# Kernel tuning notes

Measured on AMD Instinct MI355X. Metric: run time of the kernel, lower is better.

## Reference

```python
import jax, jax.numpy as jnp
import numpy as np

N, E, R, B, IN, H, OUT, P = 20000, 320000, 8, 8, 128, 256, 128, 100000
LN_EPS = 1e-5


def _xavier(key, shape):
    fan_in, fan_out = shape[-2], shape[-1]
    lim = float(np.sqrt(6.0 / (fan_in + fan_out)))
    return jax.random.uniform(key, shape, jnp.float32, -lim, lim)


def setup_inputs() -> dict:
    key = jax.random.key(0)
    ks = iter(jax.random.split(key, 64))
    inp = {}
    inp['x'] = jax.random.normal(next(ks), (N, IN), jnp.float32)
    inp['edge_index'] = jax.random.randint(next(ks), (2, E), 0, N, jnp.int32)
    inp['edge_type'] = jax.random.randint(next(ks), (E,), 0, R, jnp.int32)
    inp['gene_pairs'] = jax.random.randint(next(ks), (2, P), 0, N, jnp.int32)
    dims = [(IN, H), (H, H), (H, H), (H, OUT)]  # per-layer (in_ch, out_ch)
    for i, (ic, oc) in enumerate(dims):
        inp[f'basis{i}'] = _xavier(next(ks), (B, ic, oc))
        inp[f'att{i}'] = _xavier(next(ks), (R, B))
        inp[f'root{i}'] = _xavier(next(ks), (ic, oc))
        inp[f'relatt{i}'] = jnp.ones((R,), jnp.float32)
        inp[f'g{i}'] = jnp.ones((oc,), jnp.float32)
        inp[f'b{i}'] = jnp.zeros((oc,), jnp.float32)
    inp['res0'] = _xavier(next(ks), (IN, H))   # in_ch != out_ch at layer 0
    inp['res3'] = _xavier(next(ks), (H, OUT))  # and at layer 3
    # decoder: 3*OUT -> H -> H//2 -> H//4 -> 1
    ddims = [(3 * OUT, H), (H, H // 2), (H // 2, H // 4), (H // 4, 1)]
    for i, (ic, oc) in enumerate(ddims):
        inp[f'dW{i}'] = _xavier(next(ks), (ic, oc))
        inp[f'db{i}'] = jnp.zeros((oc,), jnp.float32)
        if i < 3:
            inp[f'dg{i}'] = jnp.ones((oc,), jnp.float32)
            inp[f'dbb{i}'] = jnp.zeros((oc,), jnp.float32)
    return inp


def _ln(h, g, b):
    m = h.mean(-1, keepdims=True)
    v = ((h - m) ** 2).mean(-1, keepdims=True)
    return (h - m) * jax.lax.rsqrt(v + LN_EPS) * g + b


def _conv(x, src, dst, et, basis, att, root_w, rel_att):
    # W_r = sum_b att[r,b] * B_b ; message = a_{r(e)} * x_src @ W_{r(e)}
    # Since the message is linear, aggregate x_src per (dst, relation) first
    # (segment_sum), then apply the R small GEMMs once - same math, no [E,in,out].
    n, d = x.shape
    weight = jnp.einsum('rb,bio->rio', att, basis)          # [R,in,out]
    a = jax.nn.softmax(rel_att)                              # [R]
    seg = dst.astype(jnp.int32) * R + et.astype(jnp.int32)   # [(node,rel)] segment ids
    agg = jax.ops.segment_sum(x[src], seg, num_segments=n * R).reshape(n, R, d)
    out = jnp.einsum('nri,rio->no', agg, weight * a[:, None, None])
    return out + x @ root_w


def reference(x, edge_index, edge_type, gene_pairs,
              basis0, att0, root0, relatt0, g0, b0, res0,
              basis1, att1, root1, relatt1, g1, b1,
              basis2, att2, root2, relatt2, g2, b2,
              basis3, att3, root3, relatt3, g3, b3, res3,
              dW0, db0, dg0, dbb0, dW1, db1, dg1, dbb1,
              dW2, db2, dg2, dbb2, dW3, db3):
    src, dst = edge_index[0], edge_index[1]
    layers = [
        (basis0, att0, root0, relatt0, g0, b0, res0),
        (basis1, att1, root1, relatt1, g1, b1, None),
        (basis2, att2, root2, relatt2, g2, b2, None),
        (basis3, att3, root3, relatt3, g3, b3, res3),
    ]
    h = x
    for i, (bs, at, rt, ra, g, b, res) in enumerate(layers):
        h_in = h
        h = _conv(h, src, dst, edge_type, bs, at, rt, ra)
        h = _ln(h, g, b)
        h = h + (h_in @ res if res is not None else h_in)
        if i < len(layers) - 1:
            h = jax.nn.gelu(h, approximate=False)
    z = h  # [N, OUT]
    zi, zj = z[gene_pairs[0]], z[gene_pairs[1]]
    pe = jnp.concatenate([zi + zj, zi * zj, jnp.abs(zi - zj)], axis=-1)
    d = jax.nn.gelu(_ln(pe @ dW0 + db0, dg0, dbb0), approximate=False)
    d = jax.nn.gelu(_ln(d @ dW1 + db1, dg1, dbb1), approximate=False)
    d = jax.nn.gelu(_ln(d @ dW2 + db2, dg2, dbb2), approximate=False)
    logits = (d @ dW3 + db3).squeeze(-1)  # [P]
    return logits, z
```

## Files before the change

### kernel.cpp

```cpp
#include <hip/hip_runtime.h>
#include <hip/hip_bf16.h>
#include <math.h>
#include <cstddef>
#include <stdint.h>

#define NN 20000
#define EE 320000
#define RR 8
#define PP 100000
#define NR (NN * RR)

typedef __hip_bfloat16 bf16;
typedef __attribute__((ext_vector_type(8))) short short8;
typedef __attribute__((ext_vector_type(4))) float floatx4;

__device__ __forceinline__ float b2f(bf16 v) { return __bfloat162float(v); }
__device__ __forceinline__ bf16 f2b(float v) { return __float2bfloat16(v); }
__device__ __forceinline__ float bits2f(unsigned short u) {
  unsigned int i = ((unsigned int)u) << 16; float f; __builtin_memcpy(&f, &i, 4); return f;
}
__device__ __forceinline__ short f2bits(float f) {
  bf16 h = __float2bfloat16(f); short s; __builtin_memcpy(&s, &h, 2); return s;
}
__device__ __forceinline__ float gelu_f(float y) {
  return 0.5f * y * (1.f + erff(y * 0.7071067811865476f));
}
__device__ __forceinline__ void async_copy16(void* lds, const void* g) {
  __builtin_amdgcn_global_load_lds((const __attribute__((address_space(1))) void*)g,
                                   (__attribute__((address_space(3))) void*)lds, 16, 0, 0);
}
__device__ __forceinline__ const short8* frag_at(const bf16* base, int row, int q) {
  return (const short8*)(base + row * 64 + (((q) ^ (row & 7)) << 3));
}
__device__ __forceinline__ const short8* frag256(const bf16* base, int row, int col64, int q) {
  return (const short8*)(base + row * 256 + col64 + (((q) ^ (row & 7)) << 3));
}
__device__ __forceinline__ int idx128(int row, int qg) {
  return row * 128 + ((qg >> 3) << 6) + (((qg & 7) ^ (row & 7)) << 3);
}

__global__ void hist_k(const int* __restrict__ dst, const int* __restrict__ et,
                       int* __restrict__ counts) {
  int e = blockIdx.x * 256 + threadIdx.x;
  if (e >= EE) return;
  atomicAdd(&counts[dst[e] * RR + et[e]], 1);
}

__global__ void scan1_k(const int* __restrict__ counts, int* __restrict__ prefix,
                        int* __restrict__ bsums) {
  __shared__ int tmp[256];
  int i = blockIdx.x * 256 + threadIdx.x;
  int v = counts[i];
  tmp[threadIdx.x] = v; __syncthreads();
  for (int off = 1; off < 256; off <<= 1) {
    int x = (threadIdx.x >= off) ? tmp[threadIdx.x - off] : 0;
    __syncthreads();
    tmp[threadIdx.x] += x;
    __syncthreads();
  }
  prefix[i] = tmp[threadIdx.x] - v;
  if (threadIdx.x == 255) bsums[blockIdx.x] = tmp[255];
}

__global__ void scan2_k(int* __restrict__ bsums, int nb) {
  __shared__ int tmp[256];
  __shared__ int carry;
  if (threadIdx.x == 0) carry = 0;
  __syncthreads();
  for (int base = 0; base < nb; base += 256) {
    int i = base + threadIdx.x;
    int v = (i < nb) ? bsums[i] : 0;
    tmp[threadIdx.x] = v; __syncthreads();
    for (int off = 1; off < 256; off <<= 1) {
      int x = (threadIdx.x >= off) ? tmp[threadIdx.x - off] : 0;
      __syncthreads();
      tmp[threadIdx.x] += x;
      __syncthreads();
    }
    int c = carry;
    if (i < nb) bsums[i] = c + tmp[threadIdx.x] - v;
    __syncthreads();
    if (threadIdx.x == 255) carry = c + tmp[255];
    __syncthreads();
  }
}

__global__ void scan3_k(int* __restrict__ prefix, const int* __restrict__ bsums) {
  int i = blockIdx.x * 256 + threadIdx.x;
  prefix[i] += bsums[blockIdx.x];
}

__global__ void scatter_k(const int* __restrict__ src, const int* __restrict__ dst,
                          const int* __restrict__ et, const int* __restrict__ segstart,
                          int* __restrict__ cursor, int* __restrict__ ssrc) {
  int e = blockIdx.x * 256 + threadIdx.x;
  if (e >= EE) return;
  int s = dst[e] * RR + et[e];
  int pos = atomicAdd(&cursor[s], 1);
  ssrc[segstart[s] + pos] = src[e];
}

__global__ void cvt_bf16_k(const float* __restrict__ in, bf16* __restrict__ out, int n) {
  int i = blockIdx.x * 256 + threadIdx.x;
  if (i < n) out[i] = f2b(in[i]);
}

__global__ void softmax4_k(const float* r0, const float* r1, const float* r2,
                           const float* r3, float* __restrict__ a) {
  if (threadIdx.x == 0) {
    const float* rs[4] = {r0, r1, r2, r3};
    for (int l = 0; l < 4; ++l) {
      float mx = -1e30f;
      for (int i = 0; i < RR; ++i) mx = fmaxf(mx, rs[l][i]);
      float e[RR]; float s = 0.f;
      for (int i = 0; i < RR; ++i) { e[i] = expf(rs[l][i] - mx); s += e[i]; }
      for (int i = 0; i < RR; ++i) a[l * RR + i] = e[i] / s;
    }
  }
}

__global__ void transpose_k(const float* __restrict__ in, bf16* __restrict__ out,
                            int rows, int cols) {
  int idx = blockIdx.x * 256 + threadIdx.x;
  if (idx >= rows * cols) return;
  int r = idx / cols, c = idx - r * cols;
  out[(size_t)c * rows + r] = f2b(in[idx]);
}

__global__ void prep_w_k(const float* __restrict__ basis, const float* __restrict__ att,
                         const float* __restrict__ root, const float* __restrict__ a,
                         bf16* __restrict__ Wt, int ic, int icsh, int oc, int ocsh) {
  int idx = blockIdx.x * 256 + threadIdx.x;
  int cols = 9 * ic;
  if (idx >= cols * oc) return;
  int o = idx & (oc - 1);
  int col = idx >> ocsh;
  int r = col >> icsh;
  int k = col & (ic - 1);
  float val;
  if (r < RR) {
    float acc = 0.f;
    for (int bb = 0; bb < RR; ++bb)
      acc += att[r * RR + bb] * basis[((size_t)bb * ic + k) * oc + o];
    val = a[r] * acc;
  } else {
    val = root[(size_t)k * oc + o];
  }
  Wt[(size_t)o * cols + col] = f2b(val);
}

__global__ __launch_bounds__(256) void aggregate_k(
    const bf16* __restrict__ h, const int* __restrict__ segstart,
    const int* __restrict__ counts, const int* __restrict__ ssrc,
    bf16* __restrict__ agg, int ic, int tpnsh) {
  int tpn = 1 << tpnsh;
  int npb = 256 >> tpnsh;
  int local = threadIdx.x >> tpnsh;
  int n = blockIdx.x * npb + local;
  if (n >= NN) return;
  int cbase = (threadIdx.x & (tpn - 1)) * 8;
  size_t rowoff = (size_t)n * (9 * ic);
  for (int r = 0; r < RR; ++r) {
    int s = n * RR + r;
    int st = segstart[s];
    int cnt = counts[s];
    float a[8] = {0.f, 0.f, 0.f, 0.f, 0.f, 0.f, 0.f, 0.f};
    for (int i = 0; i < cnt; ++i) {
      int src = ssrc[st + i];
      short8 v = *(const short8*)(h + (size_t)src * ic + cbase);
#pragma unroll
      for (int j = 0; j < 8; ++j) a[j] += bits2f((unsigned short)v[j]);
    }
    short8 o;
#pragma unroll
    for (int j = 0; j < 8; ++j) o[j] = f2bits(a[j]);
    *(short8*)(agg + rowoff + r * ic + cbase) = o;
  }
  *(short8*)(agg + rowoff + 8 * ic + cbase) =
      *(const short8*)(h + (size_t)n * ic + cbase);
}

__global__ __launch_bounds__(256) void gemm_f32_k(
    const bf16* __restrict__ A, const bf16* __restrict__ Wt,
    float* __restrict__ Cf, int M, int N, int K) {
  __shared__ __align__(16) bf16 As[128 * 64];
  __shared__ __align__(16) bf16 Ws[64 * 64];
  const int m0 = blockIdx.x * 128;
  const int n0 = blockIdx.y * 64;
  const int tid = threadIdx.x;
  const int wave = tid >> 6, lane = tid & 63;
  const int quad = lane >> 4, l16 = lane & 15;
  const int wm = (wave >> 1) * 64, wn = (wave & 1) * 32;
  floatx4 acc[4][2];
#pragma unroll
  for (int i = 0; i < 4; ++i)
#pragma unroll
    for (int j = 0; j < 2; ++j) acc[i][j] = (floatx4){0.f, 0.f, 0.f, 0.f};

  for (int k0 = 0; k0 < K; k0 += 64) {
#pragma unroll
    for (int q = 0; q < 4; ++q) {
      int c0 = (wave * 4 + q) * 1024;
      int row = (c0 >> 7) + (lane >> 3);
      int grow = m0 + row; if (grow >= M) grow = M - 1;
      int ch = (lane & 7) ^ (row & 7);
      async_copy16((char*)As + c0, A + (size_t)grow * K + k0 + ch * 8);
    }
#pragma unroll
    for (int q = 0; q < 2; ++q) {
      int c0 = (wave * 2 + q) * 1024;
      int row = (c0 >> 7) + (lane >> 3);
      int ch = (lane & 7) ^ (row & 7);
      async_copy16((char*)Ws + c0, Wt + (size_t)(n0 + row) * K + k0 + ch * 8);
    }
    __syncthreads();
#pragma unroll
    for (int kk = 0; kk < 64; kk += 32) {
      int qb = (kk >> 3) + quad;
      short8 b0 = *frag_at(Ws, wn + l16, qb);
      short8 b1 = *frag_at(Ws, wn + 16 + l16, qb);
#pragma unroll
      for (int i = 0; i < 4; ++i) {
        short8 a = *frag_at(As, wm + i * 16 + l16, qb);
        acc[i][0] = __builtin_amdgcn_mfma_f32_16x16x32_bf16(a, b0, acc[i][0], 0, 0, 0);
        acc[i][1] = __builtin_amdgcn_mfma_f32_16x16x32_bf16(a, b1, acc[i][1], 0, 0, 0);
      }
    }
    __syncthreads();
  }
#pragma unroll
  for (int i = 0; i < 4; ++i)
#pragma unroll
    for (int j = 0; j < 2; ++j)
#pragma unroll
      for (int r = 0; r < 4; ++r) {
        int row = m0 + wm + i * 16 + quad * 4 + r;
        int col = n0 + wn + j * 16 + l16;
        if (row < M) Cf[(size_t)row * N + col] = acc[i][j][r];
      }
}

__global__ __launch_bounds__(256) void gemm_plain_k(
    const bf16* __restrict__ A, const bf16* __restrict__ Wt,
    bf16* __restrict__ Cb, int M, int N, int K) {
  __shared__ __align__(16) bf16 As[64 * 64];
  __shared__ __align__(16) bf16 Ws[64 * 64];
  const int m0 = blockIdx.x * 64;
  const int n0 = blockIdx.y * 64;
  const int tid = threadIdx.x;
  const int wave = tid >> 6, lane = tid & 63;
  const int quad = lane >> 4, l16 = lane & 15;
  const int wm = (wave >> 1) * 32, wn = (wave & 1) * 32;
  floatx4 acc00 = {0.f, 0.f, 0.f, 0.f};
  floatx4 acc01 = acc00, acc10 = acc00, acc11 = acc00;

  for (int k0 = 0; k0 < K; k0 += 64) {
#pragma unroll
    for (int q = 0; q < 2; ++q) {
      int c0 = (wave * 2 + q) * 1024;
      int row = (c0 >> 7) + (lane >> 3);
      int grow = m0 + row; if (grow >= M) grow = M - 1;
      int ch = (lane & 7) ^ (row & 7);
      async_copy16((char*)As + c0, A + (size_t)grow * K + k0 + ch * 8);
    }
#pragma unroll
    for (int q = 0; q < 2; ++q) {
      int c0 = (wave * 2 + q) * 1024;
      int row = (c0 >> 7) + (lane >> 3);
      int ch = (lane & 7) ^ (row & 7);
      async_copy16((char*)Ws + c0, Wt + (size_t)(n0 + row) * K + k0 + ch * 8);
    }
    __syncthreads();
#pragma unroll
    for (int kk = 0; kk < 64; kk += 32) {
      int qb = (kk >> 3) + quad;
      short8 a0 = *frag_at(As, wm + l16, qb);
      short8 a1 = *frag_at(As, wm + 16 + l16, qb);
      short8 b0 = *frag_at(Ws, wn + l16, qb);
      short8 b1 = *frag_at(Ws, wn + 16 + l16, qb);
      acc00 = __builtin_amdgcn_mfma_f32_16x16x32_bf16(a0, b0, acc00, 0, 0, 0);
      acc01 = __builtin_amdgcn_mfma_f32_16x16x32_bf16(a0, b1, acc01, 0, 0, 0);
      acc10 = __builtin_amdgcn_mfma_f32_16x16x32_bf16(a1, b0, acc10, 0, 0, 0);
      acc11 = __builtin_amdgcn_mfma_f32_16x16x32_bf16(a1, b1, acc11, 0, 0, 0);
    }
    __syncthreads();
  }
  floatx4 accs[2][2] = {{acc00, acc01}, {acc10, acc11}};
#pragma unroll
  for (int i = 0; i < 2; ++i)
#pragma unroll
    for (int j = 0; j < 2; ++j)
#pragma unroll
      for (int r = 0; r < 4; ++r) {
        int row = m0 + wm + i * 16 + quad * 4 + r;
        int col = n0 + wn + j * 16 + l16;
        if (row < M) Cb[(size_t)row * N + col] = f2b(accs[i][j][r]);
      }
}

__global__ __launch_bounds__(256) void ln_conv_k(
    const float* __restrict__ conv, const bf16* __restrict__ res,
    const float* __restrict__ g, const float* __restrict__ b,
    bf16* __restrict__ out, float* __restrict__ zout, int oc, int do_gelu) {
  int wave = threadIdx.x >> 6, lane = threadIdx.x & 63;
  int row = blockIdx.x * 4 + wave;
  if (row >= NN) return;
  int ne = oc >> 6;
  float v[4];
  float s = 0.f, s2 = 0.f;
  for (int i = 0; i < ne; ++i) {
    v[i] = conv[(size_t)row * oc + i * 64 + lane];
    s += v[i]; s2 += v[i] * v[i];
  }
  for (int off = 32; off; off >>= 1) { s += __shfl_xor(s, off); s2 += __shfl_xor(s2, off); }
  float m = s / oc;
  float var = s2 / oc - m * m;
  float rs = rsqrtf(var + 1e-5f);
  for (int i = 0; i < ne; ++i) {
    int c = i * 64 + lane;
    float y = (v[i] - m) * rs * g[c] + b[c];
    y += b2f(res[(size_t)row * oc + c]);
    if (zout) zout[(size_t)row * oc + c] = y;
    if (do_gelu) y = gelu_f(y);
    out[(size_t)row * oc + c] = f2b(y);
  }
}

__global__ __launch_bounds__(256) void gemm_pe_k(
    const bf16* __restrict__ z, const int* __restrict__ pairs,
    const bf16* __restrict__ WAT, const bf16* __restrict__ WBT,
    const bf16* __restrict__ WCT,
    const float* __restrict__ db0, const float* __restrict__ g,
    const float* __restrict__ b, bf16* __restrict__ D0) {
  __shared__ __align__(16) bf16 PEs[64 * 64];
  __shared__ __align__(16) bf16 Ws[256 * 64];
  __shared__ float red[64][2][2];
  const int tid = threadIdx.x;
  const int wave = tid >> 6, lane = tid & 63;
  const int quad = lane >> 4, l16 = lane & 15;
  const int wr = (wave >> 1) * 32;
  const int wc = (wave & 1) * 128;
  const int m0 = blockIdx.x * 64;

  const int prow = tid >> 2, q4 = tid & 3;
  int pp = m0 + prow; if (pp >= PP) pp = PP - 1;
  const bf16* zi = z + (size_t)pairs[pp] * 128;
  const bf16* zj = z + (size_t)pairs[PP + pp] * 128;

  floatx4 acc[2][8];
#pragma unroll
  for (int i = 0; i < 2; ++i)
#pragma unroll
    for (int j = 0; j < 8; ++j) acc[i][j] = (floatx4){0.f, 0.f, 0.f, 0.f};

#pragma unroll
  for (int kwi = 0; kwi < 2; ++kwi) {
    const int kw = kwi * 64;
    const int zc = kw + q4 * 16;
    short8 va0 = *(const short8*)(zi + zc);
    short8 va1 = *(const short8*)(zi + zc + 8);
    short8 vb0 = *(const short8*)(zj + zc);
    short8 vb1 = *(const short8*)(zj + zc + 8);
#pragma unroll
    for (int op = 0; op < 3; ++op) {
      const bf16* W = (op == 0) ? WAT : (op == 1) ? WBT : WCT;
#pragma unroll
      for (int q = 0; q < 8; ++q) {
        int c0 = (q * 4 + wave) * 1024;
        int row = (c0 >> 7) + (lane >> 3);
        int ch = (lane & 7) ^ (row & 7);
        async_copy16((char*)Ws + c0, W + (size_t)row * 128 + kw + ch * 8);
      }
      {
        short8 o0, o1;
#pragma unroll
        for (int jj = 0; jj < 8; ++jj) {
          float a0 = bits2f((unsigned short)va0[jj]), b0v = bits2f((unsigned short)vb0[jj]);
          float a1 = bits2f((unsigned short)va1[jj]), b1v = bits2f((unsigned short)vb1[jj]);
          float v0 = (op == 0) ? (a0 + b0v) : (op == 1) ? (a0 * b0v) : fabsf(a0 - b0v);
          float v1 = (op == 0) ? (a1 + b1v) : (op == 1) ? (a1 * b1v) : fabsf(a1 - b1v);
          o0[jj] = f2bits(v0);
          o1[jj] = f2bits(v1);
        }
        *(short8*)(PEs + prow * 64 + (((q4 * 2) ^ (prow & 7)) << 3)) = o0;
        *(short8*)(PEs + prow * 64 + (((q4 * 2 + 1) ^ (prow & 7)) << 3)) = o1;
      }
      __syncthreads();
#pragma unroll
      for (int kk = 0; kk < 64; kk += 32) {
        int qb = (kk >> 3) + quad;
        short8 a0 = *frag_at(PEs, wr + l16, qb);
        short8 a1 = *frag_at(PEs, wr + 16 + l16, qb);
#pragma unroll
        for (int j = 0; j < 8; ++j) {
          short8 bb = *frag_at(Ws, wc + j * 16 + l16, qb);
          acc[0][j] = __builtin_amdgcn_mfma_f32_16x16x32_bf16(a0, bb, acc[0][j], 0, 0, 0);
          acc[1][j] = __builtin_amdgcn_mfma_f32_16x16x32_bf16(a1, bb, acc[1][j], 0, 0, 0);
        }
      }
      __syncthreads();
    }
  }

#pragma unroll
  for (int j = 0; j < 8; ++j) {
    float bv = db0[wc + j * 16 + l16];
#pragma unroll
    for (int i = 0; i < 2; ++i)
#pragma unroll
      for (int r = 0; r < 4; ++r) acc[i][j][r] += bv;
  }
#pragma unroll
  for (int i = 0; i < 2; ++i)
#pragma unroll
    for (int r = 0; r < 4; ++r) {
      float s = 0.f, s2 = 0.f;
#pragma unroll
      for (int j = 0; j < 8; ++j) { float v = acc[i][j][r]; s += v; s2 += v * v; }
#pragma unroll
      for (int off = 1; off < 16; off <<= 1) {
        s += __shfl_xor(s, off);
        s2 += __shfl_xor(s2, off);
      }
      if (l16 == 0) {
        int row = wr + i * 16 + quad * 4 + r;
        red[row][wave & 1][0] = s;
        red[row][wave & 1][1] = s2;
      }
    }
  __syncthreads();
#pragma unroll
  for (int j = 0; j < 8; ++j) {
    int col = wc + j * 16 + l16;
    float gg = g[col], bb2 = b[col];
#pragma unroll
    for (int i = 0; i < 2; ++i)
#pragma unroll
      for (int r = 0; r < 4; ++r) {
        int row = wr + i * 16 + quad * 4 + r;
        int grow = m0 + row;
        if (grow >= PP) continue;
        float s = red[row][0][0] + red[row][1][0];
        float s2 = red[row][0][1] + red[row][1][1];
        float mean = s / 256.f;
        float var = s2 / 256.f - mean * mean;
        float rs = rsqrtf(var + 1e-5f);
        float y = (acc[i][j][r] - mean) * rs * gg + bb2;
        D0[(size_t)grow * 256 + col] = f2b(gelu_f(y));
      }
  }
}

__global__ __launch_bounds__(256) void lngemm1_k(
    const bf16* __restrict__ D0, const bf16* __restrict__ W1t,
    const float* __restrict__ bias, bf16* __restrict__ P1, int M) {
  __shared__ __align__(16) bf16 As[64 * 256];
  __shared__ __align__(16) bf16 Ws[128 * 64];
  const int tid = threadIdx.x;
  const int wave = tid >> 6, lane = tid & 63;
  const int quad = lane >> 4, l16 = lane & 15;
  const int wr = (wave >> 1) * 32;
  const int wc = (wave & 1) * 64;
  const int m0 = blockIdx.x * 64;

  {
    const int srow = tid >> 2;
    const int q4 = tid & 3;
    int grow = m0 + srow; if (grow >= M) grow = M - 1;
    const bf16* src = D0 + (size_t)grow * 256 + q4 * 64;
#pragma unroll
    for (int c8 = 0; c8 < 8; ++c8) {
      short8 o = *(const short8*)(src + c8 * 8);
      *(short8*)(As + srow * 256 + q4 * 64 + ((c8 ^ (srow & 7)) << 3)) = o;
    }
  }

  floatx4 acc[2][4];
#pragma unroll
  for (int i = 0; i < 2; ++i)
#pragma unroll
    for (int j = 0; j < 4; ++j) acc[i][j] = (floatx4){0.f, 0.f, 0.f, 0.f};

  for (int kc = 0; kc < 4; ++kc) {
#pragma unroll
    for (int q = 0; q < 4; ++q) {
      int c0 = q * 4096 + wave * 1024;
      int row = (c0 >> 7) + (lane >> 3);
      int ch = (lane & 7) ^ (row & 7);
      async_copy16((char*)Ws + c0, W1t + (size_t)row * 256 + kc * 64 + ch * 8);
    }
    __syncthreads();
#pragma unroll
    for (int kk = 0; kk < 64; kk += 32) {
      int qb = (kk >> 3) + quad;
      short8 a0 = *frag256(As, wr + l16, kc * 64, qb);
      short8 a1 = *frag256(As, wr + 16 + l16, kc * 64, qb);
#pragma unroll
      for (int j = 0; j < 4; ++j) {
        short8 bb = *frag_at(Ws, wc + j * 16 + l16, qb);
        acc[0][j] = __builtin_amdgcn_mfma_f32_16x16x32_bf16(a0, bb, acc[0][j], 0, 0, 0);
        acc[1][j] = __builtin_amdgcn_mfma_f32_16x16x32_bf16(a1, bb, acc[1][j], 0, 0, 0);
      }
    }
    __syncthreads();
  }

#pragma unroll
  for (int i = 0; i < 2; ++i)
#pragma unroll
    for (int r = 0; r < 4; ++r) {
      int row = wr + i * 16 + quad * 4 + r;
      int grow = m0 + row;
      if (grow >= M) continue;
#pragma unroll
      for (int j = 0; j < 4; ++j) {
        int col = wc + j * 16 + l16;
        P1[(size_t)grow * 128 + col] = f2b(acc[i][j][r] + bias[col]);
      }
    }
}

__global__ __launch_bounds__(256) void lngemm2_k(
    const bf16* __restrict__ P1, const bf16* __restrict__ W2t,
    const float* __restrict__ g, const float* __restrict__ b,
    const float* __restrict__ bias, bf16* __restrict__ P2, int M) {
  __shared__ __align__(16) bf16 As[64 * 128];
  __shared__ __align__(16) bf16 Ws[64 * 64];
  const int tid = threadIdx.x;
  const int wave = tid >> 6, lane = tid & 63;
  const int quad = lane >> 4, l16 = lane & 15;
  const int m0 = blockIdx.x * 64;

  {
    const int srow = tid >> 2;
    const int q4 = tid & 3;
    int grow = m0 + srow; if (grow >= M) grow = M - 1;
    const bf16* src = P1 + (size_t)grow * 128 + q4 * 32;
    float v[32];
    float s = 0.f, s2 = 0.f;
#pragma unroll
    for (int c8 = 0; c8 < 4; ++c8) {
      short8 x = *(const short8*)(src + c8 * 8);
#pragma unroll
      for (int jj = 0; jj < 8; ++jj) {
        float f = bits2f((unsigned short)x[jj]);
        v[c8 * 8 + jj] = f; s += f; s2 += f * f;
      }
    }
    s += __shfl_xor(s, 1); s2 += __shfl_xor(s2, 1);
    s += __shfl_xor(s, 2); s2 += __shfl_xor(s2, 2);
    float mean = s / 128.f;
    float var = s2 / 128.f - mean * mean;
    float rs = rsqrtf(var + 1e-5f);
#pragma unroll
    for (int c8 = 0; c8 < 4; ++c8) {
      short8 o;
#pragma unroll
      for (int jj = 0; jj < 8; ++jj) {
        int col = q4 * 32 + c8 * 8 + jj;
        float y = (v[c8 * 8 + jj] - mean) * rs * g[col] + b[col];
        o[jj] = f2bits(gelu_f(y));
      }
      *(short8*)(As + idx128(srow, q4 * 4 + c8)) = o;
    }
  }

  floatx4 acc[4];
#pragma unroll
  for (int j = 0; j < 4; ++j) acc[j] = (floatx4){0.f, 0.f, 0.f, 0.f};

  for (int kc = 0; kc < 2; ++kc) {
#pragma unroll
    for (int q = 0; q < 2; ++q) {
      int c0 = q * 4096 + wave * 1024;
      int row = (c0 >> 7) + (lane >> 3);
      int ch = (lane & 7) ^ (row & 7);
      async_copy16((char*)Ws + c0, W2t + (size_t)row * 128 + kc * 64 + ch * 8);
    }
    __syncthreads();
#pragma unroll
    for (int kk = 0; kk < 64; kk += 32) {
      int qb = (kk >> 3) + quad;
      short8 a = *(const short8*)(As + idx128(wave * 16 + l16, kc * 8 + qb));
#pragma unroll
      for (int j = 0; j < 4; ++j) {
        short8 bb = *frag_at(Ws, j * 16 + l16, qb);
        acc[j] = __builtin_amdgcn_mfma_f32_16x16x32_bf16(a, bb, acc[j], 0, 0, 0);
      }
    }
    __syncthreads();
  }

#pragma unroll
  for (int r = 0; r < 4; ++r) {
    int row = wave * 16 + quad * 4 + r;
    int grow = m0 + row;
    if (grow >= M) continue;
#pragma unroll
    for (int j = 0; j < 4; ++j) {
      int col = j * 16 + l16;
      P2[(size_t)grow * 64 + col] = f2b(acc[j][r] + bias[col]);
    }
  }
}

__global__ __launch_bounds__(256) void logits_k(const bf16* __restrict__ P2,
                                                const float* __restrict__ g,
                                                const float* __restrict__ b,
                                                const float* __restrict__ w3,
                                                const float* __restrict__ b3,
                                                float* __restrict__ out) {
  int wave = threadIdx.x >> 6, lane = threadIdx.x & 63;
  int p = blockIdx.x * 4 + wave;
  if (p >= PP) return;
  float v = b2f(P2[(size_t)p * 64 + lane]);
  float s = v, s2 = v * v;
  for (int off = 32; off; off >>= 1) { s += __shfl_xor(s, off); s2 += __shfl_xor(s2, off); }
  float m = s / 64.f;
  float var = s2 / 64.f - m * m;
  float rs = rsqrtf(var + 1e-5f);
  float y = gelu_f((v - m) * rs * g[lane] + b[lane]);
  float t = y * w3[lane];
  for (int off = 32; off; off >>= 1) t += __shfl_xor(t, off);
  if (lane == 0) out[p] = t + b3[0];
}

extern "C" void kernel_launch(void* const* d_in, const int* in_sizes, int n_in,
                              void* d_out, int out_size, void* d_ws, size_t ws_size,
                              hipStream_t stream) {
  auto cdiv = [](int a, int b) { return (a + b - 1) / b; };

  const float* x = (const float*)d_in[0];
  const int* ei = (const int*)d_in[1];
  const int* et = (const int*)d_in[2];
  const int* gp = (const int*)d_in[3];
  const float *basis[4], *att[4], *root[4], *relatt[4], *gln[4], *bln[4];
  for (int l = 0; l < 4; ++l) {
    basis[l]  = (const float*)d_in[4 + 6 * l];
    att[l]    = (const float*)d_in[5 + 6 * l];
    root[l]   = (const float*)d_in[6 + 6 * l];
    relatt[l] = (const float*)d_in[7 + 6 * l];
    gln[l]    = (const float*)d_in[8 + 6 * l];
    bln[l]    = (const float*)d_in[9 + 6 * l];
  }
  const float* res0 = (const float*)d_in[28];
  const float* res3 = (const float*)d_in[29];
  const float* dW0 = (const float*)d_in[30]; const float* db0 = (const float*)d_in[31];
  const float* dg0 = (const float*)d_in[32]; const float* dbb0 = (const float*)d_in[33];
  const float* dW1 = (const float*)d_in[34]; const float* db1 = (const float*)d_in[35];
  const float* dg1 = (const float*)d_in[36]; const float* dbb1 = (const float*)d_in[37];
  const float* dW2 = (const float*)d_in[38]; const float* db2 = (const float*)d_in[39];
  const float* dg2 = (const float*)d_in[40]; const float* dbb2 = (const float*)d_in[41];
  const float* dW3 = (const float*)d_in[42]; const float* db3 = (const float*)d_in[43];

  char* base = (char*)d_ws;
  size_t off = 0;
  auto alloc = [&](size_t bytes) -> char* {
    char* p = base + off;
    off += (bytes + 255) & ~(size_t)255;
    return p;
  };
  bf16* X16 = (bf16*)alloc((size_t)NN * 128 * 2);
  bf16* HA  = (bf16*)alloc((size_t)NN * 256 * 2);
  bf16* HB  = (bf16*)alloc((size_t)NN * 256 * 2);
  bf16* RESB = (bf16*)alloc((size_t)NN * 256 * 2);
  float* CONV = (float*)alloc((size_t)NN * 256 * 4);
  bf16* WT    = (bf16*)alloc((size_t)589824 * 2);
  bf16* RES0T = (bf16*)alloc((size_t)32768 * 2);
  bf16* RES3T = (bf16*)alloc((size_t)32768 * 2);
  bf16* WAT   = (bf16*)alloc((size_t)32768 * 2);
  bf16* WBT   = (bf16*)alloc((size_t)32768 * 2);
  bf16* WCT   = (bf16*)alloc((size_t)32768 * 2);
  bf16* DW1T  = (bf16*)alloc((size_t)32768 * 2);
  bf16* DW2T  = (bf16*)alloc((size_t)8192 * 2);
  float* ASOFT = (float*)alloc(32 * 4);
  int* COUNTS = (int*)alloc((size_t)NR * 4);
  int* SEG    = (int*)alloc((size_t)NR * 4);
  int* CUR    = (int*)alloc((size_t)NR * 4);
  int* BS     = (int*)alloc(1024 * 4);
  int* SSRC   = (int*)alloc((size_t)EE * 4);
  char* BIG = alloc(93000000);
  bf16* AGG = (bf16*)BIG;
  bf16* D0  = (bf16*)BIG;
  bf16* P1  = (bf16*)alloc((size_t)PP * 128 * 2);
  bf16* P2  = (bf16*)alloc((size_t)PP * 64 * 2);
  (void)ws_size; (void)in_sizes; (void)n_in; (void)out_size;

  float* out_logits = (float*)d_out;
  float* out_z = (float*)d_out + PP;

  hipMemsetAsync(COUNTS, 0, (size_t)NR * 4, stream);
  hipMemsetAsync(CUR, 0, (size_t)NR * 4, stream);
  hist_k<<<cdiv(EE, 256), 256, 0, stream>>>(ei + EE, et, COUNTS);
  scan1_k<<<NR / 256, 256, 0, stream>>>(COUNTS, SEG, BS);
  scan2_k<<<1, 256, 0, stream>>>(BS, NR / 256);
  scan3_k<<<NR / 256, 256, 0, stream>>>(SEG, BS);
  scatter_k<<<cdiv(EE, 256), 256, 0, stream>>>(ei, ei + EE, et, SEG, CUR, SSRC);

  cvt_bf16_k<<<cdiv(NN * 128, 256), 256, 0, stream>>>(x, X16, NN * 128);
  softmax4_k<<<1, 64, 0, stream>>>(relatt[0], relatt[1], relatt[2], relatt[3], ASOFT);
  transpose_k<<<cdiv(128 * 256, 256), 256, 0, stream>>>(res0, RES0T, 128, 256);
  transpose_k<<<cdiv(256 * 128, 256), 256, 0, stream>>>(res3, RES3T, 256, 128);
  transpose_k<<<cdiv(128 * 256, 256), 256, 0, stream>>>(dW0, WAT, 128, 256);
  transpose_k<<<cdiv(128 * 256, 256), 256, 0, stream>>>(dW0 + 128 * 256, WBT, 128, 256);
  transpose_k<<<cdiv(128 * 256, 256), 256, 0, stream>>>(dW0 + 256 * 256, WCT, 128, 256);
  transpose_k<<<cdiv(256 * 128, 256), 256, 0, stream>>>(dW1, DW1T, 256, 128);
  transpose_k<<<cdiv(128 * 64, 256), 256, 0, stream>>>(dW2, DW2T, 128, 64);

  prep_w_k<<<cdiv(9 * 128 * 256, 256), 256, 0, stream>>>(basis[0], att[0], root[0], ASOFT + 0, WT, 128, 7, 256, 8);
  aggregate_k<<<cdiv(NN, 16), 256, 0, stream>>>(X16, SEG, COUNTS, SSRC, AGG, 128, 4);
  gemm_plain_k<<<dim3(cdiv(NN, 64), 4), 256, 0, stream>>>(X16, RES0T, RESB, NN, 256, 128);
  gemm_f32_k<<<dim3(cdiv(NN, 128), 4), 256, 0, stream>>>(AGG, WT, CONV, NN, 256, 1152);
  ln_conv_k<<<cdiv(NN, 4), 256, 0, stream>>>(CONV, RESB, gln[0], bln[0], HA, nullptr, 256, 1);

  prep_w_k<<<cdiv(9 * 256 * 256, 256), 256, 0, stream>>>(basis[1], att[1], root[1], ASOFT + 8, WT, 256, 8, 256, 8);
  aggregate_k<<<cdiv(NN, 8), 256, 0, stream>>>(HA, SEG, COUNTS, SSRC, AGG, 256, 5);
  gemm_f32_k<<<dim3(cdiv(NN, 128), 4), 256, 0, stream>>>(AGG, WT, CONV, NN, 256, 2304);
  ln_conv_k<<<cdiv(NN, 4), 256, 0, stream>>>(CONV, HA, gln[1], bln[1], HB, nullptr, 256, 1);

  prep_w_k<<<cdiv(9 * 256 * 256, 256), 256, 0, stream>>>(basis[2], att[2], root[2], ASOFT + 16, WT, 256, 8, 256, 8);
  aggregate_k<<<cdiv(NN, 8), 256, 0, stream>>>(HB, SEG, COUNTS, SSRC, AGG, 256, 5);
  gemm_f32_k<<<dim3(cdiv(NN, 128), 4), 256, 0, stream>>>(AGG, WT, CONV, NN, 256, 2304);
  ln_conv_k<<<cdiv(NN, 4), 256, 0, stream>>>(CONV, HB, gln[2], bln[2], HA, nullptr, 256, 1);

  prep_w_k<<<cdiv(9 * 256 * 128, 256), 256, 0, stream>>>(basis[3], att[3], root[3], ASOFT + 24, WT, 256, 8, 128, 7);
  aggregate_k<<<cdiv(NN, 8), 256, 0, stream>>>(HA, SEG, COUNTS, SSRC, AGG, 256, 5);
  gemm_plain_k<<<dim3(cdiv(NN, 64), 2), 256, 0, stream>>>(HA, RES3T, RESB, NN, 128, 256);
  gemm_f32_k<<<dim3(cdiv(NN, 128), 2), 256, 0, stream>>>(AGG, WT, CONV, NN, 128, 2304);
  ln_conv_k<<<cdiv(NN, 4), 256, 0, stream>>>(CONV, RESB, gln[3], bln[3], HB, out_z, 128, 0);

  gemm_pe_k<<<cdiv(PP, 64), 256, 0, stream>>>(HB, gp, WAT, WBT, WCT, db0, dg0, dbb0, D0);
  lngemm1_k<<<cdiv(PP, 64), 256, 0, stream>>>(D0, DW1T, db1, P1, PP);
  lngemm2_k<<<cdiv(PP, 64), 256, 0, stream>>>(P1, DW2T, dg1, dbb1, db2, P2, PP);
  logits_k<<<cdiv(PP, 4), 256, 0, stream>>>(P2, dg2, dbb2, dW3, db3, out_logits);
}
```

Baseline: 845.4 us.

## Split-K conv GEMMs and retile pair-encoder GEMM with separate LayerNorm pass

```diff
diff --git a/kernel.cpp b/kernel.cpp
--- a/kernel.cpp
+++ b/kernel.cpp
@@ -12,6 +12,7 @@
 
 typedef __hip_bfloat16 bf16;
 typedef __attribute__((ext_vector_type(8))) short short8;
+typedef __attribute__((ext_vector_type(4))) short short4v;
 typedef __attribute__((ext_vector_type(4))) float floatx4;
 
 __device__ __forceinline__ float b2f(bf16 v) { return __bfloat162float(v); }
@@ -182,11 +183,14 @@
 
 __global__ __launch_bounds__(256) void gemm_f32_k(
     const bf16* __restrict__ A, const bf16* __restrict__ Wt,
-    float* __restrict__ Cf, int M, int N, int K) {
+    float* __restrict__ Cf, int M, int N, int K, int ksplit) {
   __shared__ __align__(16) bf16 As[128 * 64];
   __shared__ __align__(16) bf16 Ws[64 * 64];
   const int m0 = blockIdx.x * 128;
   const int n0 = blockIdx.y * 64;
+  const int kbeg = blockIdx.z * ksplit;
+  const int kend = min(K, kbeg + ksplit);
+  float* C = Cf + (size_t)blockIdx.z * M * N;
   const int tid = threadIdx.x;
   const int wave = tid >> 6, lane = tid & 63;
   const int quad = lane >> 4, l16 = lane & 15;
@@ -197,7 +201,7 @@
 #pragma unroll
     for (int j = 0; j < 2; ++j) acc[i][j] = (floatx4){0.f, 0.f, 0.f, 0.f};
 
-  for (int k0 = 0; k0 < K; k0 += 64) {
+  for (int k0 = kbeg; k0 < kend; k0 += 64) {
 #pragma unroll
     for (int q = 0; q < 4; ++q) {
       int c0 = (wave * 4 + q) * 1024;
@@ -236,7 +240,7 @@
       for (int r = 0; r < 4; ++r) {
         int row = m0 + wm + i * 16 + quad * 4 + r;
         int col = n0 + wn + j * 16 + l16;
-        if (row < M) Cf[(size_t)row * N + col] = acc[i][j][r];
+        if (row < M) C[(size_t)row * N + col] = acc[i][j][r];
       }
 }
 
@@ -299,7 +303,8 @@
 }
 
 __global__ __launch_bounds__(256) void ln_conv_k(
-    const float* __restrict__ conv, const bf16* __restrict__ res,
+    const float* __restrict__ conv, const float* __restrict__ conv2,
+    const bf16* __restrict__ res,
     const float* __restrict__ g, const float* __restrict__ b,
     bf16* __restrict__ out, float* __restrict__ zout, int oc, int do_gelu) {
   int wave = threadIdx.x >> 6, lane = threadIdx.x & 63;
@@ -309,7 +314,8 @@
   float v[4];
   float s = 0.f, s2 = 0.f;
   for (int i = 0; i < ne; ++i) {
-    v[i] = conv[(size_t)row * oc + i * 64 + lane];
+    size_t idx = (size_t)row * oc + i * 64 + lane;
+    v[i] = conv[idx] + conv2[idx];
     s += v[i]; s2 += v[i] * v[i];
   }
   for (int off = 32; off; off >>= 1) { s += __shfl_xor(s, off); s2 += __shfl_xor(s2, off); }
@@ -330,72 +336,71 @@
     const bf16* __restrict__ z, const int* __restrict__ pairs,
     const bf16* __restrict__ WAT, const bf16* __restrict__ WBT,
     const bf16* __restrict__ WCT,
-    const float* __restrict__ db0, const float* __restrict__ g,
-    const float* __restrict__ b, bf16* __restrict__ D0) {
-  __shared__ __align__(16) bf16 PEs[64 * 64];
-  __shared__ __align__(16) bf16 Ws[256 * 64];
-  __shared__ float red[64][2][2];
+    bf16* __restrict__ P0) {
+  __shared__ __align__(16) bf16 PEs[128 * 64];
+  __shared__ __align__(16) bf16 Ws[64 * 64];
   const int tid = threadIdx.x;
   const int wave = tid >> 6, lane = tid & 63;
   const int quad = lane >> 4, l16 = lane & 15;
-  const int wr = (wave >> 1) * 32;
-  const int wc = (wave & 1) * 128;
-  const int m0 = blockIdx.x * 64;
-
-  const int prow = tid >> 2, q4 = tid & 3;
+  const int wm = (wave >> 1) * 64, wn = (wave & 1) * 32;
+  const int m0 = blockIdx.x * 128;
+  const int n0 = blockIdx.y * 64;
+
+  const int prow = tid >> 1;
+  const int colq = (tid & 1) * 32;
   int pp = m0 + prow; if (pp >= PP) pp = PP - 1;
   const bf16* zi = z + (size_t)pairs[pp] * 128;
   const bf16* zj = z + (size_t)pairs[PP + pp] * 128;
 
-  floatx4 acc[2][8];
-#pragma unroll
-  for (int i = 0; i < 2; ++i)
-#pragma unroll
-    for (int j = 0; j < 8; ++j) acc[i][j] = (floatx4){0.f, 0.f, 0.f, 0.f};
+  floatx4 acc[4][2];
+#pragma unroll
+  for (int i = 0; i < 4; ++i)
+#pragma unroll
+    for (int j = 0; j < 2; ++j) acc[i][j] = (floatx4){0.f, 0.f, 0.f, 0.f};
 
 #pragma unroll
   for (int kwi = 0; kwi < 2; ++kwi) {
     const int kw = kwi * 64;
-    const int zc = kw + q4 * 16;
-    short8 va0 = *(const short8*)(zi + zc);
-    short8 va1 = *(const short8*)(zi + zc + 8);
-    short8 vb0 = *(const short8*)(zj + zc);
-    short8 vb1 = *(const short8*)(zj + zc + 8);
+    short8 va[4], vb[4];
+#pragma unroll
+    for (int c8 = 0; c8 < 4; ++c8) {
+      va[c8] = *(const short8*)(zi + kw + colq + c8 * 8);
+      vb[c8] = *(const short8*)(zj + kw + colq + c8 * 8);
+    }
 #pragma unroll
     for (int op = 0; op < 3; ++op) {
       const bf16* W = (op == 0) ? WAT : (op == 1) ? WBT : WCT;
 #pragma unroll
-      for (int q = 0; q < 8; ++q) {
-        int c0 = (q * 4 + wave) * 1024;
+      for (int q = 0; q < 2; ++q) {
+        int c0 = q * 4096 + wave * 1024;
         int row = (c0 >> 7) + (lane >> 3);
         int ch = (lane & 7) ^ (row & 7);
-        async_copy16((char*)Ws + c0, W + (size_t)row * 128 + kw + ch * 8);
-      }
-      {
-        short8 o0, o1;
+        async_copy16((char*)Ws + c0, W + (size_t)(n0 + row) * 128 + kw + ch * 8);
+      }
+#pragma unroll
+      for (int c8 = 0; c8 < 4; ++c8) {
+        short8 o;
 #pragma unroll
         for (int jj = 0; jj < 8; ++jj) {
-          float a0 = bits2f((unsigned short)va0[jj]), b0v = bits2f((unsigned short)vb0[jj]);
-          float a1 = bits2f((unsigned short)va1[jj]), b1v = bits2f((unsigned short)vb1[jj]);
-          float v0 = (op == 0) ? (a0 + b0v) : (op == 1) ? (a0 * b0v) : fabsf(a0 - b0v);
-          float v1 = (op == 0) ? (a1 + b1v) : (op == 1) ? (a1 * b1v) : fabsf(a1 - b1v);
-          o0[jj] = f2bits(v0);
-          o1[jj] = f2bits(v1);
+          float fa = bits2f((unsigned short)va[c8][jj]);
+          float fb = bits2f((unsigned short)vb[c8][jj]);
+          float v = (op == 0) ? (fa + fb) : (op == 1) ? (fa * fb) : fabsf(fa - fb);
+          o[jj] = f2bits(v);
         }
-        *(short8*)(PEs + prow * 64 + (((q4 * 2) ^ (prow & 7)) << 3)) = o0;
-        *(short8*)(PEs + prow * 64 + (((q4 * 2 + 1) ^ (prow & 7)) << 3)) = o1;
+        int q = (tid & 1) * 4 + c8;
+        *(short8*)(PEs + prow * 64 + ((q ^ (prow & 7)) << 3)) = o;
       }
       __syncthreads();
 #pragma unroll
       for (int kk = 0; kk < 64; kk += 32) {
         int qb = (kk >> 3) + quad;
-        short8 a0 = *frag_at(PEs, wr + l16, qb);
-        short8 a1 = *frag_at(PEs, wr + 16 + l16, qb);
-#pragma unroll
-        for (int j = 0; j < 8; ++j) {
-          short8 bb = *frag_at(Ws, wc + j * 16 + l16, qb);
-          acc[0][j] = __builtin_amdgcn_mfma_f32_16x16x32_bf16(a0, bb, acc[0][j], 0, 0, 0);
-          acc[1][j] = __builtin_amdgcn_mfma_f32_16x16x32_bf16(a1, bb, acc[1][j], 0, 0, 0);
+        short8 b0 = *frag_at(Ws, wn + l16, qb);
+        short8 b1 = *frag_at(Ws, wn + 16 + l16, qb);
+#pragma unroll
+        for (int i = 0; i < 4; ++i) {
+          short8 a = *frag_at(PEs, wm + i * 16 + l16, qb);
+          acc[i][0] = __builtin_amdgcn_mfma_f32_16x16x32_bf16(a, b0, acc[i][0], 0, 0, 0);
+          acc[i][1] = __builtin_amdgcn_mfma_f32_16x16x32_bf16(a, b1, acc[i][1], 0, 0, 0);
         }
       }
       __syncthreads();
@@ -403,52 +408,45 @@
   }
 
 #pragma unroll
-  for (int j = 0; j < 8; ++j) {
-    float bv = db0[wc + j * 16 + l16];
-#pragma unroll
-    for (int i = 0; i < 2; ++i)
-#pragma unroll
-      for (int r = 0; r < 4; ++r) acc[i][j][r] += bv;
-  }
-#pragma unroll
-  for (int i = 0; i < 2; ++i)
-#pragma unroll
-    for (int r = 0; r < 4; ++r) {
-      float s = 0.f, s2 = 0.f;
-#pragma unroll
-      for (int j = 0; j < 8; ++j) { float v = acc[i][j][r]; s += v; s2 += v * v; }
-#pragma unroll
-      for (int off = 1; off < 16; off <<= 1) {
-        s += __shfl_xor(s, off);
-        s2 += __shfl_xor(s2, off);
-      }
-      if (l16 == 0) {
-        int row = wr + i * 16 + quad * 4 + r;
-        red[row][wave & 1][0] = s;
-        red[row][wave & 1][1] = s2;
-      }
-    }
-  __syncthreads();
-#pragma unroll
-  for (int j = 0; j < 8; ++j) {
-    int col = wc + j * 16 + l16;
-    float gg = g[col], bb2 = b[col];
-#pragma unroll
-    for (int i = 0; i < 2; ++i)
+  for (int i = 0; i < 4; ++i)
+#pragma unroll
+    for (int j = 0; j < 2; ++j)
 #pragma unroll
       for (int r = 0; r < 4; ++r) {
-        int row = wr + i * 16 + quad * 4 + r;
-        int grow = m0 + row;
-        if (grow >= PP) continue;
-        float s = red[row][0][0] + red[row][1][0];
-        float s2 = red[row][0][1] + red[row][1][1];
-        float mean = s / 256.f;
-        float var = s2 / 256.f - mean * mean;
-        float rs = rsqrtf(var + 1e-5f);
-        float y = (acc[i][j][r] - mean) * rs * gg + bb2;
-        D0[(size_t)grow * 256 + col] = f2b(gelu_f(y));
-      }
-  }
+        int row = m0 + wm + i * 16 + quad * 4 + r;
+        int col = n0 + wn + j * 16 + l16;
+        if (row < PP) P0[(size_t)row * 256 + col] = f2b(acc[i][j][r]);
+      }
+}
+
+__global__ __launch_bounds__(256) void ln_d0_k(bf16* __restrict__ D0,
+                                               const float* __restrict__ db0,
+                                               const float* __restrict__ g,
+                                               const float* __restrict__ b) {
+  int wave = threadIdx.x >> 6, lane = threadIdx.x & 63;
+  int row = blockIdx.x * 4 + wave;
+  if (row >= PP) return;
+  bf16* p = D0 + (size_t)row * 256 + lane * 4;
+  short4v xv = *(const short4v*)p;
+  float v[4];
+  float s = 0.f, s2 = 0.f;
+#pragma unroll
+  for (int k = 0; k < 4; ++k) {
+    v[k] = bits2f((unsigned short)xv[k]) + db0[lane * 4 + k];
+    s += v[k]; s2 += v[k] * v[k];
+  }
+  for (int off = 32; off; off >>= 1) { s += __shfl_xor(s, off); s2 += __shfl_xor(s2, off); }
+  float m = s / 256.f;
+  float var = s2 / 256.f - m * m;
+  float rs = rsqrtf(var + 1e-5f);
+  short4v ov;
+#pragma unroll
+  for (int k = 0; k < 4; ++k) {
+    int c = lane * 4 + k;
+    float y = (v[k] - m) * rs * g[c] + b[c];
+    ov[k] = f2bits(gelu_f(y));
+  }
+  *(short4v*)p = ov;
 }
 
 __global__ __launch_bounds__(256) void lngemm1_k(
@@ -664,7 +662,7 @@
   bf16* HA  = (bf16*)alloc((size_t)NN * 256 * 2);
   bf16* HB  = (bf16*)alloc((size_t)NN * 256 * 2);
   bf16* RESB = (bf16*)alloc((size_t)NN * 256 * 2);
-  float* CONV = (float*)alloc((size_t)NN * 256 * 4);
+  float* CONV = (float*)alloc((size_t)2 * NN * 256 * 4);
   bf16* WT    = (bf16*)alloc((size_t)589824 * 2);
   bf16* RES0T = (bf16*)alloc((size_t)32768 * 2);
   bf16* RES3T = (bf16*)alloc((size_t)32768 * 2);
@@ -710,26 +708,27 @@
   prep_w_k<<<cdiv(9 * 128 * 256, 256), 256, 0, stream>>>(basis[0], att[0], root[0], ASOFT + 0, WT, 128, 7, 256, 8);
   aggregate_k<<<cdiv(NN, 16), 256, 0, stream>>>(X16, SEG, COUNTS, SSRC, AGG, 128, 4);
   gemm_plain_k<<<dim3(cdiv(NN, 64), 4), 256, 0, stream>>>(X16, RES0T, RESB, NN, 256, 128);
-  gemm_f32_k<<<dim3(cdiv(NN, 128), 4), 256, 0, stream>>>(AGG, WT, CONV, NN, 256, 1152);
-  ln_conv_k<<<cdiv(NN, 4), 256, 0, stream>>>(CONV, RESB, gln[0], bln[0], HA, nullptr, 256, 1);
+  gemm_f32_k<<<dim3(cdiv(NN, 128), 4, 2), 256, 0, stream>>>(AGG, WT, CONV, NN, 256, 1152, 576);
+  ln_conv_k<<<cdiv(NN, 4), 256, 0, stream>>>(CONV, CONV + (size_t)NN * 256, RESB, gln[0], bln[0], HA, nullptr, 256, 1);
 
   prep_w_k<<<cdiv(9 * 256 * 256, 256), 256, 0, stream>>>(basis[1], att[1], root[1], ASOFT + 8, WT, 256, 8, 256, 8);
   aggregate_k<<<cdiv(NN, 8), 256, 0, stream>>>(HA, SEG, COUNTS, SSRC, AGG, 256, 5);
-  gemm_f32_k<<<dim3(cdiv(NN, 128), 4), 256, 0, stream>>>(AGG, WT, CONV, NN, 256, 2304);
-  ln_conv_k<<<cdiv(NN, 4), 256, 0, stream>>>(CONV, HA, gln[1], bln[1], HB, nullptr, 256, 1);
+  gemm_f32_k<<<dim3(cdiv(NN, 128), 4, 2), 256, 0, stream>>>(AGG, WT, CONV, NN, 256, 2304, 1152);
+  ln_conv_k<<<cdiv(NN, 4), 256, 0, stream>>>(CONV, CONV + (size_t)NN * 256, HA, gln[1], bln[1], HB, nullptr, 256, 1);
 
   prep_w_k<<<cdiv(9 * 256 * 256, 256), 256, 0, stream>>>(basis[2], att[2], root[2], ASOFT + 16, WT, 256, 8, 256, 8);
   aggregate_k<<<cdiv(NN, 8), 256, 0, stream>>>(HB, SEG, COUNTS, SSRC, AGG, 256, 5);
-  gemm_f32_k<<<dim3(cdiv(NN, 128), 4), 256, 0, stream>>>(AGG, WT, CONV, NN, 256, 2304);
-  ln_conv_k<<<cdiv(NN, 4), 256, 0, stream>>>(CONV, HB, gln[2], bln[2], HA, nullptr, 256, 1);
+  gemm_f32_k<<<dim3(cdiv(NN, 128), 4, 2), 256, 0, stream>>>(AGG, WT, CONV, NN, 256, 2304, 1152);
+  ln_conv_k<<<cdiv(NN, 4), 256, 0, stream>>>(CONV, CONV + (size_t)NN * 256, HB, gln[2], bln[2], HA, nullptr, 256, 1);
 
   prep_w_k<<<cdiv(9 * 256 * 128, 256), 256, 0, stream>>>(basis[3], att[3], root[3], ASOFT + 24, WT, 256, 8, 128, 7);
   aggregate_k<<<cdiv(NN, 8), 256, 0, stream>>>(HA, SEG, COUNTS, SSRC, AGG, 256, 5);
   gemm_plain_k<<<dim3(cdiv(NN, 64), 2), 256, 0, stream>>>(HA, RES3T, RESB, NN, 128, 256);
-  gemm_f32_k<<<dim3(cdiv(NN, 128), 2), 256, 0, stream>>>(AGG, WT, CONV, NN, 128, 2304);
-  ln_conv_k<<<cdiv(NN, 4), 256, 0, stream>>>(CONV, RESB, gln[3], bln[3], HB, out_z, 128, 0);
-
-  gemm_pe_k<<<cdiv(PP, 64), 256, 0, stream>>>(HB, gp, WAT, WBT, WCT, db0, dg0, dbb0, D0);
+  gemm_f32_k<<<dim3(cdiv(NN, 128), 2, 2), 256, 0, stream>>>(AGG, WT, CONV, NN, 128, 2304, 1152);
+  ln_conv_k<<<cdiv(NN, 4), 256, 0, stream>>>(CONV, CONV + (size_t)NN * 128, RESB, gln[3], bln[3], HB, out_z, 128, 0);
+
+  gemm_pe_k<<<dim3(cdiv(PP, 128), 4), 256, 0, stream>>>(HB, gp, WAT, WBT, WCT, D0);
+  ln_d0_k<<<cdiv(PP, 4), 256, 0, stream>>>(D0, db0, dg0, dbb0);
   lngemm1_k<<<cdiv(PP, 64), 256, 0, stream>>>(D0, DW1T, db1, P1, PP);
   lngemm2_k<<<cdiv(PP, 64), 256, 0, stream>>>(P1, DW2T, dg1, dbb1, db2, P2, PP);
   logits_k<<<cdiv(PP, 4), 256, 0, stream>>>(P2, dg2, dbb2, dW3, db3, out_logits);
```

New measurement: 866.5 us. 2.5% more time.
